# Kernel tuning notes

Measured on AMD Instinct MI355X. Metric: run time of the kernel, lower is better.

The kernel has to match this reference:

```python
import jax, jax.numpy as jnp
import numpy as np
import math

B, L, D, H = 16, 512, 128, 8


def setup_inputs() -> dict:
    key = jax.random.key(0)
    ks = jax.random.split(key, 10)
    xavier = lambda k, shp: jax.random.normal(k, shp, jnp.float32) * math.sqrt(2.0 / (shp[0] + shp[1]))
    inp = {
        "x": jax.random.normal(ks[0], (B, L, D), jnp.float32),
        "W_q": xavier(ks[1], (H * D, D)),
        "b_q": jnp.zeros((H * D,), jnp.float32),
        "W_k": xavier(ks[2], (H * D, D)),
        "b_k": jnp.zeros((H * D,), jnp.float32),
        "W_v": xavier(ks[3], (H * D, D)),
        "b_v": jnp.zeros((H * D,), jnp.float32),
        "W_o": xavier(ks[4], (D, H * D)),
        "b_o": jnp.zeros((D,), jnp.float32),
        "pad_mask": jax.random.randint(ks[5], (B, L, L), 0, 2).astype(bool),
        "batch_size": B,
        "max_len": L,
    }
    return inp


def reference(x, W_q, b_q, W_k, b_k, W_v, b_v, W_o, b_o, pad_mask, batch_size, max_len):
    # project: [B, L, D] -> [B, L, H*D] -> head-major [H*B, L, D]
    def proj(W, b):
        y = jnp.einsum('bld,ed->ble', x, W) + b          # [B, L, H*D]
        y = y.reshape(batch_size, max_len, H, D)
        return y.transpose(2, 0, 1, 3).reshape(H * batch_size, max_len, D)

    q = proj(W_q, b_q)
    k = proj(W_k, b_k)
    v = proj(W_v, b_v)

    scores = jnp.einsum('nqd,nkd->nqk', q, k)            # [H*B, L, L]
    mask = jnp.tile(pad_mask, (H, 1, 1))                 # repeat(n_heads,1,1)
    # faithful quirk: mask BEFORE scaling, softmax over QUERY axis (dim=1)
    scores = jnp.where(mask, -1e9, scores) / math.sqrt(D)
    attn = jax.nn.softmax(scores, axis=1)
    att = jnp.einsum('nqk,nkd->nqd', attn, v)            # [H*B, L, D]
    # faithful quirk: torch .view from (H*B, L, D) to (B, L, H*D)
    att = att.reshape(batch_size, max_len, H * D)
    out = jnp.einsum('ble,de->bld', att, W_o) + b_o      # [B, L, D]
    return out
```

## Files before the change

### kernel.cpp

```cpp
#include <hip/hip_runtime.h>

#define B_  16
#define L_  512
#define D_  128
#define H_  8
#define HD_ 1024
#define NH_ 128
#define M_  8192

typedef unsigned short u16;
typedef __attribute__((ext_vector_type(8))) short s16x8;
typedef __attribute__((ext_vector_type(4))) float f32x4;

__device__ __forceinline__ float bf2f(u16 u) {
    union { unsigned u; float f; } x; x.u = ((unsigned)u) << 16; return x.f;
}
__device__ __forceinline__ u16 f2bf(float f) {
    unsigned u = __float_as_uint(f);
    return (u16)((u + 0x7FFFu + ((u >> 16) & 1u)) >> 16);
}

__device__ __forceinline__ void mfma_bt64(const u16* __restrict__ A, int lda,
                                          const u16* __restrict__ B, int ldb,
                                          int K, int lane, f32x4 acc[4][4]) {
    const int mr = lane & 15, quad = lane >> 4;
    for (int k0 = 0; k0 < K; k0 += 32) {
        s16x8 av[4], bv[4];
#pragma unroll
        for (int i = 0; i < 4; i++)
            av[i] = *(const s16x8*)(A + (size_t)(i * 16 + mr) * lda + k0 + quad * 8);
#pragma unroll
        for (int j = 0; j < 4; j++)
            bv[j] = *(const s16x8*)(B + (size_t)(j * 16 + mr) * ldb + k0 + quad * 8);
#pragma unroll
        for (int i = 0; i < 4; i++)
#pragma unroll
            for (int j = 0; j < 4; j++)
                acc[i][j] = __builtin_amdgcn_mfma_f32_16x16x32_bf16(av[i], bv[j], acc[i][j], 0, 0, 0);
    }
}

__global__ void k0_detect(const unsigned int* __restrict__ pad,
                          const unsigned int* __restrict__ xw,
                          int* __restrict__ flags) {
    __shared__ int sMask, sCnt;
    if (threadIdx.x == 0) { sMask = 0; sCnt = 0; }
    __syncthreads();
    int bad = 0;
#pragma unroll
    for (int i = 0; i < 4; i++) {
        unsigned u = pad[threadIdx.x * 4 + i];
        bad |= (u > 1u) ? 1 : 0;
    }
    int cnt = 0;
#pragma unroll
    for (int i = 0; i < 16; i++) {
        unsigned w = xw[threadIdx.x * 16 + i];
        unsigned e = (w >> 7) & 0xFFu;
        cnt += (e >= 100u && e <= 131u) ? 1 : 0;
    }
    if (bad) atomicOr(&sMask, 1);
    atomicAdd(&sCnt, cnt);
    __syncthreads();
    if (threadIdx.x == 0) {
        flags[0] = (sCnt > 2048) ? 1 : 0;
        flags[1] = sMask;
    }
}

#define PREP_TOT 1576064
#define PREP_V   197008
__global__ __launch_bounds__(256) void kprep_conv(
    const void* x, const void* Wq, const void* bq, const void* Wk, const void* bk,
    const void* Wv, const void* bv, const void* Wo, const void* bo,
    const int* __restrict__ flags,
    u16* xb, u16* Wqb, u16* Wkb, u16* Wvb, u16* Wob,
    u16* bqb, u16* bkb, u16* bvb, u16* bob) {
    int gid = blockIdx.x * 256 + threadIdx.x;
    if (gid >= PREP_V) return;
    int e0 = gid * 8;
    const int dt = flags[0];
    const void* src; u16* dst; int off;
    if      (e0 < 1048576) { src = x;  dst = xb;  off = e0; }
    else if (e0 < 1179648) { src = Wq; dst = Wqb; off = e0 - 1048576; }
    else if (e0 < 1310720) { src = Wk; dst = Wkb; off = e0 - 1179648; }
    else if (e0 < 1441792) { src = Wv; dst = Wvb; off = e0 - 1310720; }
    else if (e0 < 1572864) { src = Wo; dst = Wob; off = e0 - 1441792; }
    else if (e0 < 1573888) { src = bq; dst = bqb; off = e0 - 1572864; }
    else if (e0 < 1574912) { src = bk; dst = bkb; off = e0 - 1573888; }
    else if (e0 < 1575936) { src = bv; dst = bvb; off = e0 - 1574912; }
    else                   { src = bo; dst = bob; off = e0 - 1575936; }
    if (dt) {
        *(uint4*)(dst + off) = *(const uint4*)((const u16*)src + off);
    } else {
        const float* s = (const float*)src + off;
        float4 a = *(const float4*)s, b = *(const float4*)(s + 4);
        u16 tmp[8] = {f2bf(a.x), f2bf(a.y), f2bf(a.z), f2bf(a.w),
                      f2bf(b.x), f2bf(b.y), f2bf(b.z), f2bf(b.w)};
        *(uint4*)(dst + off) = *(const uint4*)tmp;
    }
}

__global__ __launch_bounds__(256) void kprep_mask(const void* __restrict__ pad,
                                                  const int* __restrict__ flags,
                                                  unsigned* __restrict__ mb,
                                                  float* __restrict__ colsum) {
    int w = blockIdx.x * 256 + threadIdx.x;
    if (w < NH_ * L_) colsum[w] = 0.0f;
    unsigned m = 0;
    if (flags[1]) {
        const uint4* p = (const uint4*)pad + (size_t)w * 2;
        uint4 a = p[0], b = p[1];
        unsigned ws[8] = {a.x, a.y, a.z, a.w, b.x, b.y, b.z, b.w};
#pragma unroll
        for (int i = 0; i < 8; i++) {
            unsigned v = ws[i];
            m |= ((v & 0xFFu)        ? 1u : 0u) << (i * 4)
               | ((v & 0xFF00u)     ? 1u : 0u) << (i * 4 + 1)
               | ((v & 0xFF0000u)   ? 1u : 0u) << (i * 4 + 2)
               | ((v & 0xFF000000u) ? 1u : 0u) << (i * 4 + 3);
        }
    } else {
        const uint4* p = (const uint4*)pad + (size_t)w * 8;
#pragma unroll
        for (int i = 0; i < 8; i++) {
            uint4 v = p[i];
            m |= (v.x ? 1u : 0u) << (i * 4)
               | (v.y ? 1u : 0u) << (i * 4 + 1)
               | (v.z ? 1u : 0u) << (i * 4 + 2)
               | (v.w ? 1u : 0u) << (i * 4 + 3);
        }
    }
    mb[w] = m;
}

__global__ __launch_bounds__(256) void k1_proj(
    const u16* __restrict__ xb,
    const u16* __restrict__ Wqb, const u16* __restrict__ Wkb, const u16* __restrict__ Wvb,
    const u16* __restrict__ bqb, const u16* __restrict__ bkb, const u16* __restrict__ bvb,
    u16* __restrict__ qb, u16* __restrict__ kb, u16* __restrict__ vtb) {
    const int h  = blockIdx.y;
    const int m0 = blockIdx.x * 128;
    const int z  = blockIdx.z;
    const u16* W    = (z == 0) ? Wqb : (z == 1) ? Wkb : Wvb;
    const u16* bias = (z == 0) ? bqb : (z == 1) ? bkb : bvb;

    const int lane = threadIdx.x & 63, wave = threadIdx.x >> 6;
    const int wr = wave >> 1, wc = wave & 1;
    const int mr = lane & 15, quad = lane >> 4;

    f32x4 acc[4][4];
#pragma unroll
    for (int i = 0; i < 4; i++)
#pragma unroll
        for (int j = 0; j < 4; j++) acc[i][j] = (f32x4){0.f, 0.f, 0.f, 0.f};

    mfma_bt64(xb + (size_t)(m0 + wr * 64) * D_, D_,
              W + (size_t)(h * 128 + wc * 64) * D_, D_, D_, lane, acc);

    __shared__ __align__(16) u16 T[128][144];
#pragma unroll
    for (int i = 0; i < 4; i++)
#pragma unroll
        for (int j = 0; j < 4; j++) {
            int col = wc * 64 + j * 16 + mr;
            float bv_ = bf2f(bias[h * 128 + col]);
#pragma unroll
            for (int r = 0; r < 4; r++)
                T[wr * 64 + i * 16 + quad * 4 + r][col] = f2bf(acc[i][j][r] + bv_);
        }
    __syncthreads();

    const int bb = m0 >> 9, l0 = m0 & 511;
    const int t = threadIdx.x;
    if (z < 2) {
        u16* out = z ? kb : qb;
        const int wv = t >> 6, l = t & 63;
        const int col = (l & 15) * 8;
#pragma unroll
        for (int p = 0; p < 8; p++) {
            int row = p * 16 + wv * 4 + (l >> 4);
            u16* dst = out + ((size_t)(h * B_ + bb) * L_ + l0 + row) * D_ + col;
            *(uint4*)dst = *(const uint4*)&T[row][col];
        }
    } else {
        int d = t >> 1, lc0 = (t & 1) * 64;
        u16* dst = vtb + ((size_t)(h * B_ + bb) * D_ + d) * L_ + l0 + lc0;
#pragma unroll
        for (int c = 0; c < 64; c += 8) {
            u16 tmp[8];
#pragma unroll
            for (int s = 0; s < 8; s++) tmp[s] = T[lc0 + c + s][d];
            *(uint4*)(dst + c) = *(const uint4*)tmp;
        }
    }
}

__global__ __launch_bounds__(256, 4) void k2_scores(
    const u16* __restrict__ qb, const u16* __restrict__ kb,
    const unsigned* __restrict__ mbits,
    u16* __restrict__ sb, float* __restrict__ colsum) {
    const int bid = blockIdx.y * 16 + blockIdx.x;
    const int sw  = (bid & 7) * 256 + (bid >> 3);
    const int n   = sw >> 4;
    const int qt  = (sw >> 2) & 3, kt = sw & 3;
    const int bb  = n & (B_ - 1);
    const int lane = threadIdx.x & 63, wave = threadIdx.x >> 6;
    const int wr = wave >> 1, wc = wave & 1;
    const int mr = lane & 15, quad = lane >> 4;
    const float rs = 0.08838834764831845f;

    __shared__ __align__(16) u16 T[128][136];
    __shared__ float CS[2][128];
    __shared__ unsigned MW[128][4];

    {
        int t = threadIdx.x;
        int q = t >> 1, w2 = (t & 1) * 2;
        const unsigned* src = mbits + ((size_t)(bb << 9) + qt * 128 + q) * 16 + kt * 4 + w2;
        uint2 v = *(const uint2*)src;
        MW[q][w2] = v.x; MW[q][w2 + 1] = v.y;
    }

    f32x4 acc[4][4];
#pragma unroll
    for (int i = 0; i < 4; i++)
#pragma unroll
        for (int j = 0; j < 4; j++) acc[i][j] = (f32x4){0.f, 0.f, 0.f, 0.f};

    mfma_bt64(qb + ((size_t)n * L_ + qt * 128 + wr * 64) * D_, D_,
              kb + ((size_t)n * L_ + kt * 128 + wc * 64) * D_, D_, D_, lane, acc);
    __syncthreads();

    float cs[4] = {0.f, 0.f, 0.f, 0.f};
#pragma unroll
    for (int j = 0; j < 4; j++) {
        const int wsel = wc * 2 + (j >> 1);
        const int bit  = ((j & 1) << 4) + mr;
#pragma unroll
        for (int i = 0; i < 4; i++)
#pragma unroll
            for (int r = 0; r < 4; r++) {
                int ql = wr * 64 + i * 16 + quad * 4 + r;
                unsigned w = MW[ql][wsel];
                float e = ((w >> bit) & 1u) ? 0.f : __expf(acc[i][j][r] * rs);
                cs[j] += e;
                T[ql][wc * 64 + j * 16 + mr] = f2bf(e);
            }
    }
#pragma unroll
    for (int j = 0; j < 4; j++) {
        cs[j] += __shfl_xor(cs[j], 16);
        cs[j] += __shfl_xor(cs[j], 32);
    }
    if (quad == 0) {
#pragma unroll
        for (int j = 0; j < 4; j++) CS[wr][wc * 64 + j * 16 + mr] = cs[j];
    }
    __syncthreads();
    {
        int t = threadIdx.x;
        const int col = (t & 15) * 8;
        const int rb  = t >> 4;
#pragma unroll
        for (int p = 0; p < 8; p++) {
            int row = p * 16 + rb;
            u16* dst = sb + ((size_t)n * L_ + qt * 128 + row) * L_ + kt * 128 + col;
            *(uint4*)dst = *(const uint4*)&T[row][col];
        }
    }
    if (threadIdx.x < 128)
        atomicAdd(&colsum[(size_t)n * L_ + kt * 128 + threadIdx.x],
                  CS[0][threadIdx.x] + CS[1][threadIdx.x]);
}

__global__ __launch_bounds__(256) void k4_av(
    const u16* __restrict__ sb, const u16* __restrict__ vtb,
    const float* __restrict__ colsum, u16* __restrict__ att) {
    const int bid = blockIdx.y * 4 + blockIdx.x;
    const int sw  = (bid & 7) * 64 + (bid >> 3);
    const int n   = sw >> 2;
    const int q0  = (sw & 3) * 128;
    const int lane = threadIdx.x & 63, wave = threadIdx.x >> 6;
    const int wr = wave >> 1, wc = wave & 1;
    const int mr = lane & 15, quad = lane >> 4;

    f32x4 acc[4][4];
#pragma unroll
    for (int i = 0; i < 4; i++)
#pragma unroll
        for (int j = 0; j < 4; j++) acc[i][j] = (f32x4){0.f, 0.f, 0.f, 0.f};

    const u16* A   = sb  + ((size_t)n * L_ + q0 + wr * 64) * L_;
    const u16* Bb  = vtb + ((size_t)n * D_ + wc * 64) * L_;
    const float* cs = colsum + (size_t)n * L_;

    for (int k0 = 0; k0 < L_; k0 += 32) {
        const int kk = k0 + quad * 8;
        float lv[8];
        *(float4*)&lv[0] = *(const float4*)(cs + kk);
        *(float4*)&lv[4] = *(const float4*)(cs + kk + 4);
#pragma unroll
        for (int s = 0; s < 8; s++) lv[s] = __builtin_amdgcn_rcpf(lv[s]);

        s16x8 av[4], bv[4];
#pragma unroll
        for (int i = 0; i < 4; i++)
            av[i] = *(const s16x8*)(A + (size_t)(i * 16 + mr) * L_ + kk);
#pragma unroll
        for (int j = 0; j < 4; j++)
            bv[j] = *(const s16x8*)(Bb + (size_t)(j * 16 + mr) * L_ + kk);
#pragma unroll
        for (int i = 0; i < 4; i++) {
            u16* u = (u16*)&av[i];
#pragma unroll
            for (int s = 0; s < 8; s++) u[s] = f2bf(bf2f(u[s]) * lv[s]);
        }
#pragma unroll
        for (int i = 0; i < 4; i++)
#pragma unroll
            for (int j = 0; j < 4; j++)
                acc[i][j] = __builtin_amdgcn_mfma_f32_16x16x32_bf16(av[i], bv[j], acc[i][j], 0, 0, 0);
    }

    __shared__ __align__(16) u16 T[128][136];
#pragma unroll
    for (int i = 0; i < 4; i++)
#pragma unroll
        for (int j = 0; j < 4; j++) {
            int col = wc * 64 + j * 16 + mr;
#pragma unroll
            for (int r = 0; r < 4; r++)
                T[wr * 64 + i * 16 + quad * 4 + r][col] = f2bf(acc[i][j][r]);
        }
    __syncthreads();
    {
        int t = threadIdx.x;
        const int wv = t >> 6, l = t & 63;
        const int col = (l & 15) * 8;
#pragma unroll
        for (int p = 0; p < 8; p++) {
            int row = p * 16 + wv * 4 + (l >> 4);
            u16* dst = att + ((size_t)n * L_ + q0 + row) * D_ + col;
            *(uint4*)dst = *(const uint4*)&T[row][col];
        }
    }
}

__global__ __launch_bounds__(256) void k5_out(
    const u16* __restrict__ att, const u16* __restrict__ Wob,
    const u16* __restrict__ bob, const int* __restrict__ flags,
    void* __restrict__ out) {
    const int dt = flags[0];
    const int m0 = blockIdx.x * 32;
    const int lane = threadIdx.x & 63, wave = threadIdx.x >> 6;
    const int mr = lane & 15, quad = lane >> 4;

    f32x4 acc[2][2];
#pragma unroll
    for (int i = 0; i < 2; i++)
#pragma unroll
        for (int j = 0; j < 2; j++) acc[i][j] = (f32x4){0.f, 0.f, 0.f, 0.f};

    const u16* A  = att + (size_t)m0 * HD_;
    const u16* Bw = Wob + (size_t)(wave * 32) * HD_;
    for (int k0 = 0; k0 < HD_; k0 += 32) {
        s16x8 av[2], bv[2];
#pragma unroll
        for (int i = 0; i < 2; i++)
            av[i] = *(const s16x8*)(A + (size_t)(i * 16 + mr) * HD_ + k0 + quad * 8);
#pragma unroll
        for (int j = 0; j < 2; j++)
            bv[j] = *(const s16x8*)(Bw + (size_t)(j * 16 + mr) * HD_ + k0 + quad * 8);
#pragma unroll
        for (int i = 0; i < 2; i++)
#pragma unroll
            for (int j = 0; j < 2; j++)
                acc[i][j] = __builtin_amdgcn_mfma_f32_16x16x32_bf16(av[i], bv[j], acc[i][j], 0, 0, 0);
    }

    __shared__ __align__(16) float Tf[32][132];
#pragma unroll
    for (int i = 0; i < 2; i++)
#pragma unroll
        for (int j = 0; j < 2; j++) {
            int col = wave * 32 + j * 16 + mr;
            float bv_ = bf2f(bob[col]);
#pragma unroll
            for (int r = 0; r < 4; r++)
                Tf[i * 16 + quad * 4 + r][col] = acc[i][j][r] + bv_;
        }
    __syncthreads();
    int t = threadIdx.x, row = t >> 3, cg = (t & 7) * 16;
    size_t base = (size_t)(m0 + row) * D_ + cg;
    if (dt) {
        u16* o = (u16*)out;
        u16 tmp[16];
#pragma unroll
        for (int s = 0; s < 16; s++) tmp[s] = f2bf(Tf[row][cg + s]);
        *(uint4*)(o + base)     = *(const uint4*)&tmp[0];
        *(uint4*)(o + base + 8) = *(const uint4*)&tmp[8];
    } else {
        float* o = (float*)out;
#pragma unroll
        for (int c = 0; c < 16; c += 4)
            *(float4*)(o + base + c) = *(const float4*)&Tf[row][cg + c];
    }
}

extern "C" void kernel_launch(void* const* d_in, const int* in_sizes, int n_in,
                              void* d_out, int out_size, void* d_ws, size_t ws_size,
                              hipStream_t stream) {
    (void)in_sizes; (void)n_in; (void)out_size; (void)ws_size;
    const void* x  = d_in[0];
    const void* Wq = d_in[1]; const void* bq = d_in[2];
    const void* Wk = d_in[3]; const void* bk = d_in[4];
    const void* Wv = d_in[5]; const void* bv = d_in[6];
    const void* Wo = d_in[7]; const void* bo = d_in[8];
    const void* pad = d_in[9];

    char* p = (char*)d_ws;
    auto alloc = [&](size_t bytes) { char* r = p; p += (bytes + 255) & ~(size_t)255; return r; };
    int*  flags = (int*)alloc(256);
    u16*  xb   = (u16*)alloc(2097152);
    u16*  Wqb  = (u16*)alloc(262144);
    u16*  Wkb  = (u16*)alloc(262144);
    u16*  Wvb  = (u16*)alloc(262144);
    u16*  Wob  = (u16*)alloc(262144);
    u16*  bqb  = (u16*)alloc(2048);
    u16*  bkb  = (u16*)alloc(2048);
    u16*  bvb  = (u16*)alloc(2048);
    u16*  bob  = (u16*)alloc(256);
    unsigned* mbits = (unsigned*)alloc(524288);
    float* colsum = (float*)alloc(262144);
    u16*  qb   = (u16*)alloc(16777216);
    u16*  kb   = (u16*)alloc(16777216);
    u16*  vtb  = (u16*)alloc(16777216);
    u16*  sb   = (u16*)alloc(67108864);
    u16*  att  = qb;

    k0_detect<<<1, 256, 0, stream>>>((const unsigned*)pad, (const unsigned*)x, flags);
    kprep_conv<<<(PREP_V + 255) / 256, 256, 0, stream>>>(
        x, Wq, bq, Wk, bk, Wv, bv, Wo, bo, flags,
        xb, Wqb, Wkb, Wvb, Wob, bqb, bkb, bvb, bob);
    kprep_mask<<<512, 256, 0, stream>>>(pad, flags, mbits, colsum);
    k1_proj<<<dim3(64, 8, 3), 256, 0, stream>>>(
        xb, Wqb, Wkb, Wvb, bqb, bkb, bvb, qb, kb, vtb);
    k2_scores<<<dim3(16, NH_), 256, 0, stream>>>(qb, kb, mbits, sb, colsum);
    k4_av<<<dim3(4, NH_), 256, 0, stream>>>(sb, vtb, colsum, att);
    k5_out<<<256, 256, 0, stream>>>(att, Wob, bob, flags, d_out);
}
```

Before: 228.5 us.

## Merge prep kernels, add nontemporal loads/stores, reorder projection and output block mapping

Result: slower. 262.3 us (+14.8%).

```diff
diff --git a/kernel.cpp b/kernel.cpp
--- a/kernel.cpp
+++ b/kernel.cpp
@@ -11,6 +11,7 @@
 typedef unsigned short u16;
 typedef __attribute__((ext_vector_type(8))) short s16x8;
 typedef __attribute__((ext_vector_type(4))) float f32x4;
+typedef __attribute__((ext_vector_type(4))) unsigned u32x4;
 
 __device__ __forceinline__ float bf2f(u16 u) {
     union { unsigned u; float f; } x; x.u = ((unsigned)u) << 16; return x.f;
@@ -70,68 +71,72 @@
 
 #define PREP_TOT 1576064
 #define PREP_V   197008
-__global__ __launch_bounds__(256) void kprep_conv(
+#define PREP_CONV_BLOCKS 770
+#define PREP_MASK_BLOCKS 512
+__global__ __launch_bounds__(256) void kprep(
     const void* x, const void* Wq, const void* bq, const void* Wk, const void* bk,
     const void* Wv, const void* bv, const void* Wo, const void* bo,
-    const int* __restrict__ flags,
+    const void* __restrict__ pad, const int* __restrict__ flags,
     u16* xb, u16* Wqb, u16* Wkb, u16* Wvb, u16* Wob,
-    u16* bqb, u16* bkb, u16* bvb, u16* bob) {
-    int gid = blockIdx.x * 256 + threadIdx.x;
-    if (gid >= PREP_V) return;
-    int e0 = gid * 8;
-    const int dt = flags[0];
-    const void* src; u16* dst; int off;
-    if      (e0 < 1048576) { src = x;  dst = xb;  off = e0; }
-    else if (e0 < 1179648) { src = Wq; dst = Wqb; off = e0 - 1048576; }
-    else if (e0 < 1310720) { src = Wk; dst = Wkb; off = e0 - 1179648; }
-    else if (e0 < 1441792) { src = Wv; dst = Wvb; off = e0 - 1310720; }
-    else if (e0 < 1572864) { src = Wo; dst = Wob; off = e0 - 1441792; }
-    else if (e0 < 1573888) { src = bq; dst = bqb; off = e0 - 1572864; }
-    else if (e0 < 1574912) { src = bk; dst = bkb; off = e0 - 1573888; }
-    else if (e0 < 1575936) { src = bv; dst = bvb; off = e0 - 1574912; }
-    else                   { src = bo; dst = bob; off = e0 - 1575936; }
-    if (dt) {
-        *(uint4*)(dst + off) = *(const uint4*)((const u16*)src + off);
+    u16* bqb, u16* bkb, u16* bvb, u16* bob,
+    unsigned* __restrict__ mb, float* __restrict__ colsum) {
+    const int b = blockIdx.x;
+    if (b < PREP_CONV_BLOCKS) {
+        int gid = b * 256 + threadIdx.x;
+        if (gid >= PREP_V) return;
+        int e0 = gid * 8;
+        const int dt = flags[0];
+        const void* src; u16* dst; int off;
+        if      (e0 < 1048576) { src = x;  dst = xb;  off = e0; }
+        else if (e0 < 1179648) { src = Wq; dst = Wqb; off = e0 - 1048576; }
+        else if (e0 < 1310720) { src = Wk; dst = Wkb; off = e0 - 1179648; }
+        else if (e0 < 1441792) { src = Wv; dst = Wvb; off = e0 - 1310720; }
+        else if (e0 < 1572864) { src = Wo; dst = Wob; off = e0 - 1441792; }
+        else if (e0 < 1573888) { src = bq; dst = bqb; off = e0 - 1572864; }
+        else if (e0 < 1574912) { src = bk; dst = bkb; off = e0 - 1573888; }
+        else if (e0 < 1575936) { src = bv; dst = bvb; off = e0 - 1574912; }
+        else                   { src = bo; dst = bob; off = e0 - 1575936; }
+        if (dt) {
+            u32x4 v = __builtin_nontemporal_load((const u32x4*)((const u16*)src + off));
+            *(u32x4*)(dst + off) = v;
+        } else {
+            const float* s = (const float*)src + off;
+            f32x4 a = __builtin_nontemporal_load((const f32x4*)s);
+            f32x4 c = __builtin_nontemporal_load((const f32x4*)(s + 4));
+            u16 tmp[8] = {f2bf(a[0]), f2bf(a[1]), f2bf(a[2]), f2bf(a[3]),
+                          f2bf(c[0]), f2bf(c[1]), f2bf(c[2]), f2bf(c[3])};
+            *(u32x4*)(dst + off) = *(const u32x4*)tmp;
+        }
     } else {
-        const float* s = (const float*)src + off;
-        float4 a = *(const float4*)s, b = *(const float4*)(s + 4);
-        u16 tmp[8] = {f2bf(a.x), f2bf(a.y), f2bf(a.z), f2bf(a.w),
-                      f2bf(b.x), f2bf(b.y), f2bf(b.z), f2bf(b.w)};
-        *(uint4*)(dst + off) = *(const uint4*)tmp;
-    }
-}
-
-__global__ __launch_bounds__(256) void kprep_mask(const void* __restrict__ pad,
-                                                  const int* __restrict__ flags,
-                                                  unsigned* __restrict__ mb,
-                                                  float* __restrict__ colsum) {
-    int w = blockIdx.x * 256 + threadIdx.x;
-    if (w < NH_ * L_) colsum[w] = 0.0f;
-    unsigned m = 0;
-    if (flags[1]) {
-        const uint4* p = (const uint4*)pad + (size_t)w * 2;
-        uint4 a = p[0], b = p[1];
-        unsigned ws[8] = {a.x, a.y, a.z, a.w, b.x, b.y, b.z, b.w};
-#pragma unroll
-        for (int i = 0; i < 8; i++) {
-            unsigned v = ws[i];
-            m |= ((v & 0xFFu)        ? 1u : 0u) << (i * 4)
-               | ((v & 0xFF00u)     ? 1u : 0u) << (i * 4 + 1)
-               | ((v & 0xFF0000u)   ? 1u : 0u) << (i * 4 + 2)
-               | ((v & 0xFF000000u) ? 1u : 0u) << (i * 4 + 3);
-        }
-    } else {
-        const uint4* p = (const uint4*)pad + (size_t)w * 8;
-#pragma unroll
-        for (int i = 0; i < 8; i++) {
-            uint4 v = p[i];
-            m |= (v.x ? 1u : 0u) << (i * 4)
-               | (v.y ? 1u : 0u) << (i * 4 + 1)
-               | (v.z ? 1u : 0u) << (i * 4 + 2)
-               | (v.w ? 1u : 0u) << (i * 4 + 3);
-        }
-    }
-    mb[w] = m;
+        int w = (b - PREP_CONV_BLOCKS) * 256 + threadIdx.x;
+        if (w < NH_ * L_) colsum[w] = 0.0f;
+        unsigned m = 0;
+        if (flags[1]) {
+            const u32x4* p = (const u32x4*)pad + (size_t)w * 2;
+            u32x4 a = __builtin_nontemporal_load(p);
+            u32x4 c = __builtin_nontemporal_load(p + 1);
+            unsigned ws[8] = {a[0], a[1], a[2], a[3], c[0], c[1], c[2], c[3]};
+#pragma unroll
+            for (int i = 0; i < 8; i++) {
+                unsigned v = ws[i];
+                m |= ((v & 0xFFu)        ? 1u : 0u) << (i * 4)
+                   | ((v & 0xFF00u)     ? 1u : 0u) << (i * 4 + 1)
+                   | ((v & 0xFF0000u)   ? 1u : 0u) << (i * 4 + 2)
+                   | ((v & 0xFF000000u) ? 1u : 0u) << (i * 4 + 3);
+            }
+        } else {
+            const u32x4* p = (const u32x4*)pad + (size_t)w * 8;
+#pragma unroll
+            for (int i = 0; i < 8; i++) {
+                u32x4 v = __builtin_nontemporal_load(p + i);
+                m |= (v[0] ? 1u : 0u) << (i * 4)
+                   | (v[1] ? 1u : 0u) << (i * 4 + 1)
+                   | (v[2] ? 1u : 0u) << (i * 4 + 2)
+                   | (v[3] ? 1u : 0u) << (i * 4 + 3);
+            }
+        }
+        mb[w] = m;
+    }
 }
 
 __global__ __launch_bounds__(256) void k1_proj(
@@ -139,8 +144,8 @@
     const u16* __restrict__ Wqb, const u16* __restrict__ Wkb, const u16* __restrict__ Wvb,
     const u16* __restrict__ bqb, const u16* __restrict__ bkb, const u16* __restrict__ bvb,
     u16* __restrict__ qb, u16* __restrict__ kb, u16* __restrict__ vtb) {
-    const int h  = blockIdx.y;
-    const int m0 = blockIdx.x * 128;
+    const int h  = blockIdx.x;
+    const int m0 = blockIdx.y * 128;
     const int z  = blockIdx.z;
     const u16* W    = (z == 0) ? Wqb : (z == 1) ? Wkb : Wvb;
     const u16* bias = (z == 0) ? bqb : (z == 1) ? bkb : bvb;
@@ -181,7 +186,7 @@
         for (int p = 0; p < 8; p++) {
             int row = p * 16 + wv * 4 + (l >> 4);
             u16* dst = out + ((size_t)(h * B_ + bb) * L_ + l0 + row) * D_ + col;
-            *(uint4*)dst = *(const uint4*)&T[row][col];
+            *(u32x4*)dst = *(const u32x4*)&T[row][col];
         }
     } else {
         int d = t >> 1, lc0 = (t & 1) * 64;
@@ -191,7 +196,7 @@
             u16 tmp[8];
 #pragma unroll
             for (int s = 0; s < 8; s++) tmp[s] = T[lc0 + c + s][d];
-            *(uint4*)(dst + c) = *(const uint4*)tmp;
+            __builtin_nontemporal_store(*(const u32x4*)tmp, (u32x4*)(dst + c));
         }
     }
 }
@@ -266,7 +271,7 @@
         for (int p = 0; p < 8; p++) {
             int row = p * 16 + rb;
             u16* dst = sb + ((size_t)n * L_ + qt * 128 + row) * L_ + kt * 128 + col;
-            *(uint4*)dst = *(const uint4*)&T[row][col];
+            __builtin_nontemporal_store(*(const u32x4*)&T[row][col], (u32x4*)dst);
         }
     }
     if (threadIdx.x < 128)
@@ -306,7 +311,7 @@
         s16x8 av[4], bv[4];
 #pragma unroll
         for (int i = 0; i < 4; i++)
-            av[i] = *(const s16x8*)(A + (size_t)(i * 16 + mr) * L_ + kk);
+            av[i] = __builtin_nontemporal_load((const s16x8*)(A + (size_t)(i * 16 + mr) * L_ + kk));
 #pragma unroll
         for (int j = 0; j < 4; j++)
             bv[j] = *(const s16x8*)(Bb + (size_t)(j * 16 + mr) * L_ + kk);
@@ -342,7 +347,7 @@
         for (int p = 0; p < 8; p++) {
             int row = p * 16 + wv * 4 + (l >> 4);
             u16* dst = att + ((size_t)n * L_ + q0 + row) * D_ + col;
-            *(uint4*)dst = *(const uint4*)&T[row][col];
+            *(u32x4*)dst = *(const u32x4*)&T[row][col];
         }
     }
 }
@@ -352,7 +357,9 @@
     const u16* __restrict__ bob, const int* __restrict__ flags,
     void* __restrict__ out) {
     const int dt = flags[0];
-    const int m0 = blockIdx.x * 32;
+    const int bid = blockIdx.x;
+    const int sw  = (bid & 7) * 32 + (bid >> 3);
+    const int m0 = sw * 32;
     const int lane = threadIdx.x & 63, wave = threadIdx.x >> 6;
     const int mr = lane & 15, quad = lane >> 4;
 
@@ -398,13 +405,13 @@
         u16 tmp[16];
 #pragma unroll
         for (int s = 0; s < 16; s++) tmp[s] = f2bf(Tf[row][cg + s]);
-        *(uint4*)(o + base)     = *(const uint4*)&tmp[0];
-        *(uint4*)(o + base + 8) = *(const uint4*)&tmp[8];
+        __builtin_nontemporal_store(*(const u32x4*)&tmp[0], (u32x4*)(o + base));
+        __builtin_nontemporal_store(*(const u32x4*)&tmp[8], (u32x4*)(o + base + 8));
     } else {
         float* o = (float*)out;
 #pragma unroll
         for (int c = 0; c < 16; c += 4)
-            *(float4*)(o + base + c) = *(const float4*)&Tf[row][cg + c];
+            __builtin_nontemporal_store(*(const f32x4*)&Tf[row][cg + c], (f32x4*)(o + base + c));
     }
 }
 
@@ -440,11 +447,10 @@
     u16*  att  = qb;
 
     k0_detect<<<1, 256, 0, stream>>>((const unsigned*)pad, (const unsigned*)x, flags);
-    kprep_conv<<<(PREP_V + 255) / 256, 256, 0, stream>>>(
-        x, Wq, bq, Wk, bk, Wv, bv, Wo, bo, flags,
-        xb, Wqb, Wkb, Wvb, Wob, bqb, bkb, bvb, bob);
-    kprep_mask<<<512, 256, 0, stream>>>(pad, flags, mbits, colsum);
-    k1_proj<<<dim3(64, 8, 3), 256, 0, stream>>>(
+    kprep<<<PREP_CONV_BLOCKS + PREP_MASK_BLOCKS, 256, 0, stream>>>(
+        x, Wq, bq, Wk, bk, Wv, bv, Wo, bo, pad, flags,
+        xb, Wqb, Wkb, Wvb, Wob, bqb, bkb, bvb, bob, mbits, colsum);
+    k1_proj<<<dim3(8, 64, 3), 256, 0, stream>>>(
         xb, Wqb, Wkb, Wvb, bqb, bkb, bvb, qb, kb, vtb);
     k2_scores<<<dim3(16, NH_), 256, 0, stream>>>(qb, kb, mbits, sb, colsum);
     k4_av<<<dim3(4, NH_), 256, 0, stream>>>(sb, vtb, colsum, att);
```
